# Performance work log

Measured on AMD Instinct MI355X. Metric: run time of the kernel, lower is better.

## Reference

```python
import jax, jax.numpy as jnp
import numpy as np

REG = 0.01          # regularisation (target epsilon)
DECAY = 0.9         # decay_rate
MIN_UPDATE = 0.01   # min_update_size
MAX_ITERS = 50      # max_iterations
GRAD_CLIP = 1.0     # transport_gradient_clip
B, N, D = 4, 2048, 16


@jax.custom_vjp
def clip_grad_identity(t):
    # identity fwd; clips the cotangent of the transport matrix in bwd
    return t

def _cg_fwd(t):
    return t, None

def _cg_bwd(_, dt):
    return (jnp.clip(dt, -GRAD_CLIP, GRAD_CLIP),)

clip_grad_identity.defvjp(_cg_fwd, _cg_bwd)


def _diameter(x):
    # max over dims of per-sample std (ddof=0), per batch -> (B,1)
    d = jnp.max(jnp.std(x, axis=1), axis=-1, keepdims=True)
    return jnp.where(d == 0.0, jnp.ones_like(d), d)


def _sq_cdist(x):
    # squared euclidean auto-distance matrix, (B,N,N)
    sq = jnp.sum(x * x, axis=-1)
    c = sq[:, :, None] + sq[:, None, :] - 2.0 * jnp.einsum('bnd,bmd->bnm', x, x)
    return jnp.maximum(c, 0.0)


def sinkhorn_loop(log_a, log_b, cost, eps_target, min_update, max_iter, eps0, rate):
    """Log-domain Sinkhorn with per-batch exponentially decayed epsilon and
    masked early stopping (data-dependent stop expressed as a convergence mask
    so the loop is jit/vjp friendly). eps0: (B,1,1) initial regularisation
    (extent of the scaled particles, per Thornton & Corenflos)."""
    Bb, _ = log_a.shape
    init = (jnp.zeros_like(log_a), jnp.zeros_like(log_b), eps0,
            jnp.zeros((Bb, 1), dtype=bool))

    @jax.checkpoint
    def step(carry, _):
        f, g, eps, done = carry              # eps: (B,1,1), done: (B,1)
        eps2 = eps[:, :, 0]                  # (B,1)
        # f_i = -eps * LSE_j( log_b_j + (g_j - C_ij)/eps )
        f_new = -eps2 * jax.nn.logsumexp(log_b[:, None, :] + (g[:, None, :] - cost) / eps, axis=-1)
        cT = jnp.swapaxes(cost, 1, 2)
        # g_j = -eps * LSE_i( log_a_i + (f_i - C_ij)/eps )
        g_new = -eps2 * jax.nn.logsumexp(log_a[:, None, :] + (f_new[:, None, :] - cT) / eps, axis=-1)
        upd = jnp.maximum(jnp.max(jnp.abs(f_new - f), axis=-1),
                          jnp.max(jnp.abs(g_new - g), axis=-1))[:, None]  # (B,1)
        converged = (upd < min_update) & (eps2 <= eps_target)
        f = jnp.where(done, f, f_new)
        g = jnp.where(done, g, g_new)
        eps = jnp.where(done[:, :, None], eps, jnp.maximum(eps * rate, eps_target))
        done = done | converged
        return (f, g, eps, done), None

    (f, g, eps, _), _ = jax.lax.scan(step, init, None, length=max_iter)
    return f, g, eps


def _forward(state, weight):
    n = state.shape[1]
    log_b = jnp.full(weight.shape, -jnp.log(float(n)), weight.dtype)  # log uniform
    centred = state - jax.lax.stop_gradient(jnp.mean(state, axis=1, keepdims=True))
    scale = jax.lax.stop_gradient(_diameter(state)) * jnp.sqrt(float(state.shape[-1]))  # (B,1)
    sx = centred / scale[:, :, None]
    cost = _sq_cdist(sx)                                              # (B,N,N)
    extent = (jnp.max(sx, axis=(1, 2)) - jnp.min(sx, axis=(1, 2))).reshape(-1, 1, 1)
    f, g, _ = sinkhorn_loop(weight, log_b, cost, REG, MIN_UPDATE, MAX_ITERS, extent, DECAY)
    # transport from potentials at the target regularisation
    log_T = weight[:, :, None] + log_b[:, None, :] + (f[:, :, None] + g[:, None, :] - cost) / REG
    transport = clip_grad_identity(jnp.exp(log_T))                    # (B,N,N)
    # new particle m = N * sum_n T_nm x_n
    new_state = float(n) * jnp.einsum('bnm,bnd->bmd', transport, state)
    return new_state


def setup_inputs() -> dict:
    key = jax.random.key(0)
    k1, k2 = jax.random.split(key)
    state = jax.random.normal(k1, (B, N, D), dtype=jnp.float32)
    weight = jax.nn.log_softmax(jax.random.normal(k2, (B, N), dtype=jnp.float32), axis=-1)
    return {"state": state, "weight": weight}


def reference(state, weight):
    new_state = _forward(state, weight)
    uniform_log_w = jnp.full(weight.shape, -jnp.log(float(weight.shape[1])), weight.dtype)
    return (new_state, uniform_log_w)
```

## Files before the change

### kernel.cpp

```cpp
#include <hip/hip_runtime.h>

#define BATCH 4
#define NPTS  2048
#define DIM   16
#define REGEPS 0.01f
#define DECAYF 0.9f
#define MINUPD 0.01f
#define MAXIT  50
#define LOGN   7.62461898616f

#define OFF_SX    0
#define OFF_SQ    (BATCH*NPTS*DIM)
#define OFF_F     (OFF_SQ + BATCH*NPTS)
#define OFF_G     (OFF_F + BATCH*NPTS)
#define OFF_MEAN  (OFF_G + BATCH*NPTS)
#define OFF_SCALE (OFF_MEAN + BATCH*DIM)
#define OFF_EPS0  (OFF_SCALE + BATCH)
#define OFF_UPD   (OFF_EPS0 + BATCH)
#define OFF_DONE  (OFF_UPD + BATCH)
#define OFF_CNT   (OFF_DONE + BATCH)

__global__ __launch_bounds__(256) void ot_preproc(const float* __restrict__ state,
                                                  float* __restrict__ ws) {
  const int b = blockIdx.x;
  const int tid = threadIdx.x;
  __shared__ float s_sum[16][17];
  __shared__ float s_sq[16][17];
  __shared__ float s_mean[16];
  __shared__ float s_red[8];
  __shared__ float s_scale_sh;

  const float* st = state + b * NPTS * DIM;
  const int d = tid & 15, grp = tid >> 4;
  float sm = 0.f, s2 = 0.f;
  for (int n = grp; n < NPTS; n += 16) {
    float x = st[n * DIM + d];
    sm += x; s2 += x * x;
  }
  s_sum[grp][d] = sm; s_sq[grp][d] = s2;
  __syncthreads();
  if (tid < 16) {
    float S = 0.f, Q = 0.f;
    for (int g2 = 0; g2 < 16; ++g2) { S += s_sum[g2][tid]; Q += s_sq[g2][tid]; }
    float mean = S * (1.0f / NPTS);
    float var  = fmaxf(Q * (1.0f / NPTS) - mean * mean, 0.f);
    float sd   = sqrtf(var);
    s_mean[tid] = mean;
    ws[OFF_MEAN + b * DIM + tid] = mean;
    s_sum[0][tid] = sd;
  }
  __syncthreads();
  if (tid == 0) {
    float dm = 0.f;
    for (int d2 = 0; d2 < 16; ++d2) dm = fmaxf(dm, s_sum[0][d2]);
    if (dm == 0.f) dm = 1.f;
    float scale = dm * 4.0f;
    s_scale_sh = scale;
    ws[OFF_SCALE + b] = scale;
  }
  __syncthreads();

  const float inv_scale = 1.0f / s_scale_sh;
  float vmin = 3.0e38f, vmax = -3.0e38f;
  float* sx = ws + OFF_SX + b * NPTS * DIM;
  float* sq = ws + OFF_SQ + b * NPTS;
  for (int n = tid; n < NPTS; n += 256) {
    const float4* rp = (const float4*)(st + n * DIM);
    float4 xs0 = rp[0], xs1 = rp[1], xs2 = rp[2], xs3 = rp[3];
    float xv[16] = {xs0.x,xs0.y,xs0.z,xs0.w, xs1.x,xs1.y,xs1.z,xs1.w,
                    xs2.x,xs2.y,xs2.z,xs2.w, xs3.x,xs3.y,xs3.z,xs3.w};
    float ov[16];
    float q = 0.f;
    #pragma unroll
    for (int e = 0; e < 16; ++e) {
      float v = (xv[e] - s_mean[e]) * inv_scale;
      ov[e] = v; q += v * v;
      vmin = fminf(vmin, v); vmax = fmaxf(vmax, v);
    }
    float4* op = (float4*)(sx + n * DIM);
    op[0] = make_float4(ov[0],ov[1],ov[2],ov[3]);
    op[1] = make_float4(ov[4],ov[5],ov[6],ov[7]);
    op[2] = make_float4(ov[8],ov[9],ov[10],ov[11]);
    op[3] = make_float4(ov[12],ov[13],ov[14],ov[15]);
    sq[n] = q;
  }
  float* fv = ws + OFF_F + b * NPTS;
  float* gv = ws + OFF_G + b * NPTS;
  for (int n = tid; n < NPTS; n += 256) { fv[n] = 0.f; gv[n] = 0.f; }
  #pragma unroll
  for (int off = 32; off > 0; off >>= 1) {
    vmin = fminf(vmin, __shfl_xor(vmin, off));
    vmax = fmaxf(vmax, __shfl_xor(vmax, off));
  }
  const int wv = tid >> 6, ln = tid & 63;
  if (ln == 0) { s_red[wv] = vmin; s_red[4 + wv] = vmax; }
  __syncthreads();
  if (tid == 0) {
    float mn = fminf(fminf(s_red[0], s_red[1]), fminf(s_red[2], s_red[3]));
    float mx = fmaxf(fmaxf(s_red[4], s_red[5]), fmaxf(s_red[6], s_red[7]));
    ws[OFF_EPS0 + b] = mx - mn;
    ((unsigned int*)ws)[OFF_UPD + b] = 0u;
    ((int*)ws)[OFF_DONE + b] = 0;
  }
  if (b == 0 && tid < 64) ((int*)ws)[OFF_CNT + tid] = 0;
}

__global__ __launch_bounds__(256) void ot_pass(float* __restrict__ ws,
                                               const float* __restrict__ wlog,
                                               int it, int isF) {
  __shared__ float s_xt[DIM][256];
  __shared__ float s_a[256];
  __shared__ float s_q[256];

  const int bid = blockIdx.x;
  const int b  = bid >> 7;
  const int rb = bid & 127;
  const int tid = threadIdx.x;
  const int w = tid >> 6, l = tid & 63;

  if (!((const int*)ws)[OFF_DONE + b]) {
    float e = ws[OFF_EPS0 + b];
    #pragma unroll 1
    for (int t = 0; t < it; ++t) e = fmaxf(e * DECAYF, REGEPS);
    const float inv_e = 1.0f / e;

    const float* __restrict__ sx = ws + OFF_SX + b * NPTS * DIM;
    const float* __restrict__ sq = ws + OFF_SQ + b * NPTS;
    float* fv = ws + OFF_F + b * NPTS;
    float* gv = ws + OFF_G + b * NPTS;
    const float* __restrict__ wl = wlog + b * NPTS;

    const int row0 = rb * 16 + w * 4;
    float sxi[4][DIM], ci[4], m[4], ssum[4];
    #pragma unroll
    for (int r = 0; r < 4; ++r) {
      const int i = row0 + r;
      ci[r] = sq[i];
      const float4* rp = (const float4*)(sx + i * DIM);
      #pragma unroll
      for (int c4 = 0; c4 < 4; ++c4) {
        float4 t = rp[c4];
        sxi[r][c4*4+0] = -2.0f * t.x; sxi[r][c4*4+1] = -2.0f * t.y;
        sxi[r][c4*4+2] = -2.0f * t.z; sxi[r][c4*4+3] = -2.0f * t.w;
      }
      m[r] = -3.0e38f; ssum[r] = 0.0f;
    }

    const float* __restrict__ src = isF ? gv : fv;
    for (int k = 0; k < NPTS / 256; ++k) {
      __syncthreads();
      {
        const int j = k * 256 + tid;
        const float4* rp = (const float4*)(sx + j * DIM);
        float4 t0 = rp[0], t1 = rp[1], t2 = rp[2], t3 = rp[3];
        s_xt[0][tid]=t0.x;  s_xt[1][tid]=t0.y;  s_xt[2][tid]=t0.z;  s_xt[3][tid]=t0.w;
        s_xt[4][tid]=t1.x;  s_xt[5][tid]=t1.y;  s_xt[6][tid]=t1.z;  s_xt[7][tid]=t1.w;
        s_xt[8][tid]=t2.x;  s_xt[9][tid]=t2.y;  s_xt[10][tid]=t2.z; s_xt[11][tid]=t2.w;
        s_xt[12][tid]=t3.x; s_xt[13][tid]=t3.y; s_xt[14][tid]=t3.z; s_xt[15][tid]=t3.w;
        s_q[tid] = sq[j];
        float aj = src[j] * inv_e;
        if (!isF) aj += wl[j];
        s_a[tid] = aj;
      }
      __syncthreads();
      const float4 av = *(const float4*)&s_a[4 * l];
      const float4 qv = *(const float4*)&s_q[4 * l];
      float acc[4][4];
      #pragma unroll
      for (int r = 0; r < 4; ++r) {
        acc[r][0] = ci[r] + qv.x; acc[r][1] = ci[r] + qv.y;
        acc[r][2] = ci[r] + qv.z; acc[r][3] = ci[r] + qv.w;
      }
      #pragma unroll
      for (int dd = 0; dd < DIM; ++dd) {
        const float4 xj = *(const float4*)&s_xt[dd][4 * l];
        #pragma unroll
        for (int r = 0; r < 4; ++r) {
          const float xr = sxi[r][dd];
          acc[r][0] = fmaf(xr, xj.x, acc[r][0]);
          acc[r][1] = fmaf(xr, xj.y, acc[r][1]);
          acc[r][2] = fmaf(xr, xj.z, acc[r][2]);
          acc[r][3] = fmaf(xr, xj.w, acc[r][3]);
        }
      }
      #pragma unroll
      for (int r = 0; r < 4; ++r) {
        float v0 = fmaf(fmaxf(acc[r][0], 0.0f), -inv_e, av.x);
        float v1 = fmaf(fmaxf(acc[r][1], 0.0f), -inv_e, av.y);
        float v2 = fmaf(fmaxf(acc[r][2], 0.0f), -inv_e, av.z);
        float v3 = fmaf(fmaxf(acc[r][3], 0.0f), -inv_e, av.w);
        float cmx = fmaxf(fmaxf(v0, v1), fmaxf(v2, v3));
        float nm = fmaxf(m[r], cmx);
        float e0 = __expf(m[r] - nm);
        float sadd = __expf(v0-nm) + __expf(v1-nm) + __expf(v2-nm) + __expf(v3-nm);
        ssum[r] = fmaf(ssum[r], e0, sadd);
        m[r] = nm;
      }
    }
    #pragma unroll
    for (int off = 1; off < 64; off <<= 1) {
      #pragma unroll
      for (int r = 0; r < 4; ++r) {
        float om = __shfl_xor(m[r], off);
        float os = __shfl_xor(ssum[r], off);
        float nm = fmaxf(m[r], om);
        ssum[r] = fmaf(ssum[r], __expf(m[r]-nm), os * __expf(om-nm));
        m[r] = nm;
      }
    }
    if (l < 4) {
      const int r = l;
      float L = m[r] + __logf(ssum[r]);
      if (isF) L -= LOGN;
      const float nv = -e * L;
      float* dst = isF ? fv : gv;
      const int i = row0 + r;
      const float old = dst[i];
      dst[i] = nv;
      atomicMax((unsigned int*)ws + OFF_UPD + b, __float_as_uint(fabsf(nv - old)));
    }
  }

  if (!isF) {
    __syncthreads();
    if (tid == 0) {
      __threadfence();
      const int old = atomicAdd((int*)ws + OFF_CNT + it, 1);
      if (old == (int)gridDim.x - 1) {
        __threadfence();
        #pragma unroll 1
        for (int bb = 0; bb < BATCH; ++bb) {
          if (!((int*)ws)[OFF_DONE + bb]) {
            float u = __uint_as_float(atomicMax((unsigned int*)ws + OFF_UPD + bb, 0u));
            float e2 = ws[OFF_EPS0 + bb];
            #pragma unroll 1
            for (int t = 0; t < it; ++t) e2 = fmaxf(e2 * DECAYF, REGEPS);
            if (u < MINUPD && e2 <= REGEPS) ((int*)ws)[OFF_DONE + bb] = 1;
          }
          ((unsigned int*)ws)[OFF_UPD + bb] = 0u;
        }
        __threadfence();
      }
    }
  }
}

__global__ __launch_bounds__(256) void ot_out(float* __restrict__ ws,
                                              const float* __restrict__ wlog,
                                              float* __restrict__ out) {
  __shared__ float s_xt[DIM][256];
  __shared__ float s_p[256];
  __shared__ float s_q[256];
  const int bid = blockIdx.x;
  const int b  = bid >> 8;
  const int rb = bid & 255;
  const int tid = threadIdx.x;
  const int w = tid >> 6, l = tid & 63;
  const float invR = 1.0f / REGEPS;

  const float* __restrict__ sx = ws + OFF_SX + b * NPTS * DIM;
  const float* __restrict__ sq = ws + OFF_SQ + b * NPTS;
  const float* __restrict__ fv = ws + OFF_F + b * NPTS;
  const float* __restrict__ gv = ws + OFF_G + b * NPTS;
  const float* __restrict__ wl = wlog + b * NPTS;

  const int row0 = rb * 8 + w * 2;
  float sxm[2][DIM], cm2[2], qm[2], acc[2][DIM], accT[2];
  #pragma unroll
  for (int r = 0; r < 2; ++r) {
    const int mrow = row0 + r;
    cm2[r] = sq[mrow];
    qm[r]  = gv[mrow] * invR;
    const float4* rp = (const float4*)(sx + mrow * DIM);
    #pragma unroll
    for (int c4 = 0; c4 < 4; ++c4) {
      float4 t = rp[c4];
      sxm[r][c4*4+0] = -2.0f * t.x; sxm[r][c4*4+1] = -2.0f * t.y;
      sxm[r][c4*4+2] = -2.0f * t.z; sxm[r][c4*4+3] = -2.0f * t.w;
    }
    #pragma unroll
    for (int dd = 0; dd < DIM; ++dd) acc[r][dd] = 0.0f;
    accT[r] = 0.0f;
  }

  for (int k = 0; k < NPTS / 256; ++k) {
    __syncthreads();
    {
      const int n = k * 256 + tid;
      const float4* rp = (const float4*)(sx + n * DIM);
      float4 t0 = rp[0], t1 = rp[1], t2 = rp[2], t3 = rp[3];
      s_xt[0][tid]=t0.x;  s_xt[1][tid]=t0.y;  s_xt[2][tid]=t0.z;  s_xt[3][tid]=t0.w;
      s_xt[4][tid]=t1.x;  s_xt[5][tid]=t1.y;  s_xt[6][tid]=t1.z;  s_xt[7][tid]=t1.w;
      s_xt[8][tid]=t2.x;  s_xt[9][tid]=t2.y;  s_xt[10][tid]=t2.z; s_xt[11][tid]=t2.w;
      s_xt[12][tid]=t3.x; s_xt[13][tid]=t3.y; s_xt[14][tid]=t3.z; s_xt[15][tid]=t3.w;
      s_q[tid] = sq[n];
      s_p[tid] = wl[n] - LOGN + fv[n] * invR;
    }
    __syncthreads();
    const float4 pv = *(const float4*)&s_p[4 * l];
    const float4 qv = *(const float4*)&s_q[4 * l];
    float a2[2][4];
    #pragma unroll
    for (int r = 0; r < 2; ++r) {
      a2[r][0] = cm2[r] + qv.x; a2[r][1] = cm2[r] + qv.y;
      a2[r][2] = cm2[r] + qv.z; a2[r][3] = cm2[r] + qv.w;
    }
    #pragma unroll
    for (int dd = 0; dd < DIM; ++dd) {
      const float4 xj = *(const float4*)&s_xt[dd][4 * l];
      #pragma unroll
      for (int r = 0; r < 2; ++r) {
        const float xr = sxm[r][dd];
        a2[r][0] = fmaf(xr, xj.x, a2[r][0]);
        a2[r][1] = fmaf(xr, xj.y, a2[r][1]);
        a2[r][2] = fmaf(xr, xj.z, a2[r][2]);
        a2[r][3] = fmaf(xr, xj.w, a2[r][3]);
      }
    }
    float T[2][4];
    #pragma unroll
    for (int r = 0; r < 2; ++r) {
      T[r][0] = __expf(fmaf(fmaxf(a2[r][0], 0.f), -invR, pv.x + qm[r]));
      T[r][1] = __expf(fmaf(fmaxf(a2[r][1], 0.f), -invR, pv.y + qm[r]));
      T[r][2] = __expf(fmaf(fmaxf(a2[r][2], 0.f), -invR, pv.z + qm[r]));
      T[r][3] = __expf(fmaf(fmaxf(a2[r][3], 0.f), -invR, pv.w + qm[r]));
      accT[r] += (T[r][0] + T[r][1]) + (T[r][2] + T[r][3]);
    }
    #pragma unroll
    for (int dd = 0; dd < DIM; ++dd) {
      const float4 xj = *(const float4*)&s_xt[dd][4 * l];
      #pragma unroll
      for (int r = 0; r < 2; ++r) {
        float t = acc[r][dd];
        t = fmaf(T[r][0], xj.x, t);
        t = fmaf(T[r][1], xj.y, t);
        t = fmaf(T[r][2], xj.z, t);
        t = fmaf(T[r][3], xj.w, t);
        acc[r][dd] = t;
      }
    }
  }
  #pragma unroll
  for (int off = 1; off < 64; off <<= 1) {
    #pragma unroll
    for (int r = 0; r < 2; ++r) {
      #pragma unroll
      for (int dd = 0; dd < DIM; ++dd) acc[r][dd] += __shfl_xor(acc[r][dd], off);
      accT[r] += __shfl_xor(accT[r], off);
    }
  }
  if (l == 0) {
    const float scale = ws[OFF_SCALE + b];
    const float* mean = ws + OFF_MEAN + b * DIM;
    #pragma unroll
    for (int r = 0; r < 2; ++r) {
      const int mrow = row0 + r;
      float ov[16];
      #pragma unroll
      for (int dd = 0; dd < DIM; ++dd)
        ov[dd] = (float)NPTS * fmaf(scale, acc[r][dd], mean[dd] * accT[r]);
      float4* op = (float4*)(out + (b * NPTS + mrow) * DIM);
      op[0] = make_float4(ov[0],ov[1],ov[2],ov[3]);
      op[1] = make_float4(ov[4],ov[5],ov[6],ov[7]);
      op[2] = make_float4(ov[8],ov[9],ov[10],ov[11]);
      op[3] = make_float4(ov[12],ov[13],ov[14],ov[15]);
    }
  }
  if (tid < 8) out[BATCH * NPTS * DIM + b * NPTS + rb * 8 + tid] = -LOGN;
}

extern "C" void kernel_launch(void* const* d_in, const int* in_sizes, int n_in,
                              void* d_out, int out_size, void* d_ws, size_t ws_size,
                              hipStream_t stream) {
  (void)in_sizes; (void)n_in; (void)out_size; (void)ws_size;
  const float* state  = (const float*)d_in[0];
  const float* weight = (const float*)d_in[1];
  float* out = (float*)d_out;
  float* ws  = (float*)d_ws;

  ot_preproc<<<dim3(BATCH), dim3(256), 0, stream>>>(state, ws);
  for (int it = 0; it < MAXIT; ++it) {
    ot_pass<<<dim3(BATCH * NPTS / 16), dim3(256), 0, stream>>>(ws, weight, it, 1);
    ot_pass<<<dim3(BATCH * NPTS / 16), dim3(256), 0, stream>>>(ws, weight, it, 0);
  }
  ot_out<<<dim3(BATCH * NPTS / 8), dim3(256), 0, stream>>>(ws, weight, out);
}
```

Baseline: 4.105 ms.

## Fuse Sinkhorn iterations into one persistent cooperative kernel with per-batch grid barriers

Measured after the change: 7.464 ms. +81.9%, slower.

```diff
diff --git a/kernel.cpp b/kernel.cpp
--- a/kernel.cpp
+++ b/kernel.cpp
@@ -8,6 +8,8 @@
 #define MINUPD 0.01f
 #define MAXIT  50
 #define LOGN   7.62461898616f
+#define L2E    1.44269504089f
+#define LN2    0.69314718056f
 
 #define OFF_SX    0
 #define OFF_SQ    (BATCH*NPTS*DIM)
@@ -16,9 +18,8 @@
 #define OFF_MEAN  (OFF_G + BATCH*NPTS)
 #define OFF_SCALE (OFF_MEAN + BATCH*DIM)
 #define OFF_EPS0  (OFF_SCALE + BATCH)
-#define OFF_UPD   (OFF_EPS0 + BATCH)
-#define OFF_DONE  (OFF_UPD + BATCH)
-#define OFF_CNT   (OFF_DONE + BATCH)
+#define OFF_ARR   (OFF_EPS0 + BATCH)
+#define OFF_UPD2  (OFF_ARR + BATCH)
 
 __global__ __launch_bounds__(256) void ot_preproc(const float* __restrict__ state,
                                                   float* __restrict__ ws) {
@@ -99,148 +100,207 @@
     float mn = fminf(fminf(s_red[0], s_red[1]), fminf(s_red[2], s_red[3]));
     float mx = fmaxf(fmaxf(s_red[4], s_red[5]), fmaxf(s_red[6], s_red[7]));
     ws[OFF_EPS0 + b] = mx - mn;
-    ((unsigned int*)ws)[OFF_UPD + b] = 0u;
-    ((int*)ws)[OFF_DONE + b] = 0;
-  }
-  if (b == 0 && tid < 64) ((int*)ws)[OFF_CNT + tid] = 0;
-}
-
-__global__ __launch_bounds__(256) void ot_pass(float* __restrict__ ws,
-                                               const float* __restrict__ wlog,
-                                               int it, int isF) {
-  __shared__ float s_xt[DIM][256];
-  __shared__ float s_a[256];
-  __shared__ float s_q[256];
+    ((unsigned int*)ws)[OFF_UPD2 + 2*b + 0] = 0u;
+    ((unsigned int*)ws)[OFF_UPD2 + 2*b + 1] = 0u;
+    ((int*)ws)[OFF_ARR + b] = 0;
+  }
+}
+
+__device__ __forceinline__ void batch_barrier(int* arr, int target) {
+  __syncthreads();
+  if (threadIdx.x == 0) {
+    __hip_atomic_fetch_add(arr, 1, __ATOMIC_ACQ_REL, __HIP_MEMORY_SCOPE_AGENT);
+    while (__hip_atomic_load(arr, __ATOMIC_ACQUIRE, __HIP_MEMORY_SCOPE_AGENT) < target)
+      __builtin_amdgcn_s_sleep(8);
+  }
+  __syncthreads();
+}
+
+__device__ __forceinline__ void lse_sweep(const float* __restrict__ s_xt,
+                                          const float* __restrict__ s_a2,
+                                          const float (&sxs)[4][16],
+                                          float (&M)[4], float (&S)[4], int l) {
+  #pragma unroll
+  for (int r = 0; r < 4; ++r) { M[r] = -3.0e38f; S[r] = 0.0f; }
+  for (int c = 0; c < 8; ++c) {
+    const int jb = c * 256 + 4 * l;
+    const float4 av = *(const float4*)(s_a2 + jb);
+    float acc[4][4];
+    {
+      const float4 xj = *(const float4*)(s_xt + jb);
+      #pragma unroll
+      for (int r = 0; r < 4; ++r) {
+        acc[r][0] = fmaf(sxs[r][0], xj.x, av.x);
+        acc[r][1] = fmaf(sxs[r][0], xj.y, av.y);
+        acc[r][2] = fmaf(sxs[r][0], xj.z, av.z);
+        acc[r][3] = fmaf(sxs[r][0], xj.w, av.w);
+      }
+    }
+    #pragma unroll
+    for (int dd = 1; dd < 16; ++dd) {
+      const float4 xj = *(const float4*)(s_xt + dd * 2048 + jb);
+      #pragma unroll
+      for (int r = 0; r < 4; ++r) {
+        acc[r][0] = fmaf(sxs[r][dd], xj.x, acc[r][0]);
+        acc[r][1] = fmaf(sxs[r][dd], xj.y, acc[r][1]);
+        acc[r][2] = fmaf(sxs[r][dd], xj.z, acc[r][2]);
+        acc[r][3] = fmaf(sxs[r][dd], xj.w, acc[r][3]);
+      }
+    }
+    #pragma unroll
+    for (int r = 0; r < 4; ++r) {
+      const float cmx = fmaxf(fmaxf(acc[r][0], acc[r][1]), fmaxf(acc[r][2], acc[r][3]));
+      const float nm = fmaxf(M[r], cmx);
+      const float e0 = exp2f(M[r] - nm);
+      const float sa = exp2f(acc[r][0]-nm) + exp2f(acc[r][1]-nm)
+                     + exp2f(acc[r][2]-nm) + exp2f(acc[r][3]-nm);
+      S[r] = fmaf(S[r], e0, sa);
+      M[r] = nm;
+    }
+  }
+}
+
+__device__ __forceinline__ void lse_butterfly(float (&M)[4], float (&S)[4]) {
+  #pragma unroll
+  for (int off = 1; off < 64; off <<= 1) {
+    #pragma unroll
+    for (int r = 0; r < 4; ++r) {
+      const float om = __shfl_xor(M[r], off);
+      const float os = __shfl_xor(S[r], off);
+      const float nm = fmaxf(M[r], om);
+      S[r] = S[r] * exp2f(M[r] - nm) + os * exp2f(om - nm);
+      M[r] = nm;
+    }
+  }
+}
+
+__global__ __launch_bounds__(512, 2) void ot_sinkhorn(float* __restrict__ ws,
+                                                      const float* __restrict__ wlog) {
+  extern __shared__ float lds[];
+  float* s_xt  = lds;
+  float* s_a2  = lds + 16 * 2048;
+  float* s_wl2 = s_a2 + 2048;
 
   const int bid = blockIdx.x;
-  const int b  = bid >> 7;
-  const int rb = bid & 127;
+  const int b  = bid >> 6;
+  const int rb = bid & 63;
   const int tid = threadIdx.x;
   const int w = tid >> 6, l = tid & 63;
 
-  if (!((const int*)ws)[OFF_DONE + b]) {
-    float e = ws[OFF_EPS0 + b];
-    #pragma unroll 1
-    for (int t = 0; t < it; ++t) e = fmaxf(e * DECAYF, REGEPS);
-    const float inv_e = 1.0f / e;
-
-    const float* __restrict__ sx = ws + OFF_SX + b * NPTS * DIM;
-    const float* __restrict__ sq = ws + OFF_SQ + b * NPTS;
-    float* fv = ws + OFF_F + b * NPTS;
-    float* gv = ws + OFF_G + b * NPTS;
-    const float* __restrict__ wl = wlog + b * NPTS;
-
-    const int row0 = rb * 16 + w * 4;
-    float sxi[4][DIM], ci[4], m[4], ssum[4];
-    #pragma unroll
-    for (int r = 0; r < 4; ++r) {
-      const int i = row0 + r;
-      ci[r] = sq[i];
-      const float4* rp = (const float4*)(sx + i * DIM);
-      #pragma unroll
-      for (int c4 = 0; c4 < 4; ++c4) {
-        float4 t = rp[c4];
-        sxi[r][c4*4+0] = -2.0f * t.x; sxi[r][c4*4+1] = -2.0f * t.y;
-        sxi[r][c4*4+2] = -2.0f * t.z; sxi[r][c4*4+3] = -2.0f * t.w;
-      }
-      m[r] = -3.0e38f; ssum[r] = 0.0f;
-    }
-
-    const float* __restrict__ src = isF ? gv : fv;
-    for (int k = 0; k < NPTS / 256; ++k) {
-      __syncthreads();
-      {
-        const int j = k * 256 + tid;
-        const float4* rp = (const float4*)(sx + j * DIM);
-        float4 t0 = rp[0], t1 = rp[1], t2 = rp[2], t3 = rp[3];
-        s_xt[0][tid]=t0.x;  s_xt[1][tid]=t0.y;  s_xt[2][tid]=t0.z;  s_xt[3][tid]=t0.w;
-        s_xt[4][tid]=t1.x;  s_xt[5][tid]=t1.y;  s_xt[6][tid]=t1.z;  s_xt[7][tid]=t1.w;
-        s_xt[8][tid]=t2.x;  s_xt[9][tid]=t2.y;  s_xt[10][tid]=t2.z; s_xt[11][tid]=t2.w;
-        s_xt[12][tid]=t3.x; s_xt[13][tid]=t3.y; s_xt[14][tid]=t3.z; s_xt[15][tid]=t3.w;
-        s_q[tid] = sq[j];
-        float aj = src[j] * inv_e;
-        if (!isF) aj += wl[j];
-        s_a[tid] = aj;
-      }
-      __syncthreads();
-      const float4 av = *(const float4*)&s_a[4 * l];
-      const float4 qv = *(const float4*)&s_q[4 * l];
-      float acc[4][4];
-      #pragma unroll
-      for (int r = 0; r < 4; ++r) {
-        acc[r][0] = ci[r] + qv.x; acc[r][1] = ci[r] + qv.y;
-        acc[r][2] = ci[r] + qv.z; acc[r][3] = ci[r] + qv.w;
-      }
-      #pragma unroll
-      for (int dd = 0; dd < DIM; ++dd) {
-        const float4 xj = *(const float4*)&s_xt[dd][4 * l];
+  const float* __restrict__ sx = ws + OFF_SX + b * NPTS * DIM;
+  const float* __restrict__ sq = ws + OFF_SQ + b * NPTS;
+  float* fv = ws + OFF_F + b * NPTS;
+  float* gv = ws + OFF_G + b * NPTS;
+  const float* __restrict__ wl = wlog + b * NPTS;
+  int* arr = (int*)ws + OFF_ARR + b;
+  unsigned int* up2 = (unsigned int*)ws + OFF_UPD2 + 2 * b;
+
+  for (int j = tid; j < NPTS; j += 512) {
+    const float4* rp = (const float4*)(sx + j * DIM);
+    float4 t0 = rp[0], t1 = rp[1], t2 = rp[2], t3 = rp[3];
+    s_xt[ 0*2048+j]=t0.x; s_xt[ 1*2048+j]=t0.y; s_xt[ 2*2048+j]=t0.z; s_xt[ 3*2048+j]=t0.w;
+    s_xt[ 4*2048+j]=t1.x; s_xt[ 5*2048+j]=t1.y; s_xt[ 6*2048+j]=t1.z; s_xt[ 7*2048+j]=t1.w;
+    s_xt[ 8*2048+j]=t2.x; s_xt[ 9*2048+j]=t2.y; s_xt[10*2048+j]=t2.z; s_xt[11*2048+j]=t2.w;
+    s_xt[12*2048+j]=t3.x; s_xt[13*2048+j]=t3.y; s_xt[14*2048+j]=t3.z; s_xt[15*2048+j]=t3.w;
+    s_wl2[j] = wl[j] * L2E;
+  }
+  const int row0 = rb * 32 + w * 4;
+  float sxs[4][16];
+  #pragma unroll
+  for (int r = 0; r < 4; ++r) {
+    const float4* rp = (const float4*)(sx + (row0 + r) * DIM);
+    float4 t0 = rp[0], t1 = rp[1], t2 = rp[2], t3 = rp[3];
+    sxs[r][0]=t0.x;  sxs[r][1]=t0.y;  sxs[r][2]=t0.z;  sxs[r][3]=t0.w;
+    sxs[r][4]=t1.x;  sxs[r][5]=t1.y;  sxs[r][6]=t1.z;  sxs[r][7]=t1.w;
+    sxs[r][8]=t2.x;  sxs[r][9]=t2.y;  sxs[r][10]=t2.z; sxs[r][11]=t2.w;
+    sxs[r][12]=t3.x; sxs[r][13]=t3.y; sxs[r][14]=t3.z; sxs[r][15]=t3.w;
+  }
+  float eps = ws[OFF_EPS0 + b];
+  {
+    const float s2e0 = 2.0f * L2E / eps;
+    #pragma unroll
+    for (int r = 0; r < 4; ++r)
+      #pragma unroll
+      for (int dd = 0; dd < 16; ++dd) sxs[r][dd] *= s2e0;
+  }
+  __syncthreads();
+
+  int ph = 0;
+  for (int it = 0; it < MAXIT; ++it) {
+    const float le   = L2E / eps;
+    const float eln2 = eps * LN2;
+
+    {
+      const int j4 = tid * 4;
+      const float g0 = __hip_atomic_load(gv + j4 + 0, __ATOMIC_RELAXED, __HIP_MEMORY_SCOPE_AGENT);
+      const float g1 = __hip_atomic_load(gv + j4 + 1, __ATOMIC_RELAXED, __HIP_MEMORY_SCOPE_AGENT);
+      const float g2 = __hip_atomic_load(gv + j4 + 2, __ATOMIC_RELAXED, __HIP_MEMORY_SCOPE_AGENT);
+      const float g3 = __hip_atomic_load(gv + j4 + 3, __ATOMIC_RELAXED, __HIP_MEMORY_SCOPE_AGENT);
+      const float4 qj = *(const float4*)(sq + j4);
+      *(float4*)(s_a2 + j4) = make_float4((g0 - qj.x) * le, (g1 - qj.y) * le,
+                                          (g2 - qj.z) * le, (g3 - qj.w) * le);
+    }
+    __syncthreads();
+    {
+      float M[4], S[4];
+      lse_sweep(s_xt, s_a2, sxs, M, S, l);
+      lse_butterfly(M, S);
+      if (l < 4) {
+        const float Mr = (l==0)?M[0]:(l==1)?M[1]:(l==2)?M[2]:M[3];
+        const float Sr = (l==0)?S[0]:(l==1)?S[1]:(l==2)?S[2]:S[3];
+        const int i = row0 + l;
+        const float qi = sq[i];
+        const float fnew = fmaf(eps, LOGN, qi) - eln2 * (Mr + log2f(Sr));
+        const float old = __hip_atomic_load(fv + i, __ATOMIC_RELAXED, __HIP_MEMORY_SCOPE_AGENT);
+        __hip_atomic_store(fv + i, fnew, __ATOMIC_RELEASE, __HIP_MEMORY_SCOPE_AGENT);
+        __hip_atomic_fetch_max(up2 + (it & 1), __float_as_uint(fabsf(fnew - old)),
+                               __ATOMIC_RELAXED, __HIP_MEMORY_SCOPE_AGENT);
+      }
+    }
+    ++ph; batch_barrier(arr, 64 * ph);
+
+    if (rb == 0 && tid == 0)
+      __hip_atomic_store(up2 + ((it + 1) & 1), 0u, __ATOMIC_RELAXED, __HIP_MEMORY_SCOPE_AGENT);
+    {
+      const int j4 = tid * 4;
+      const float f0 = __hip_atomic_load(fv + j4 + 0, __ATOMIC_RELAXED, __HIP_MEMORY_SCOPE_AGENT);
+      const float f1 = __hip_atomic_load(fv + j4 + 1, __ATOMIC_RELAXED, __HIP_MEMORY_SCOPE_AGENT);
+      const float f2 = __hip_atomic_load(fv + j4 + 2, __ATOMIC_RELAXED, __HIP_MEMORY_SCOPE_AGENT);
+      const float f3 = __hip_atomic_load(fv + j4 + 3, __ATOMIC_RELAXED, __HIP_MEMORY_SCOPE_AGENT);
+      const float4 qj = *(const float4*)(sq + j4);
+      const float4 w2 = *(const float4*)(s_wl2 + j4);
+      *(float4*)(s_a2 + j4) = make_float4(fmaf(f0 - qj.x, le, w2.x), fmaf(f1 - qj.y, le, w2.y),
+                                          fmaf(f2 - qj.z, le, w2.z), fmaf(f3 - qj.w, le, w2.w));
+    }
+    __syncthreads();
+    {
+      float M[4], S[4];
+      lse_sweep(s_xt, s_a2, sxs, M, S, l);
+      lse_butterfly(M, S);
+      if (l < 4) {
+        const float Mr = (l==0)?M[0]:(l==1)?M[1]:(l==2)?M[2]:M[3];
+        const float Sr = (l==0)?S[0]:(l==1)?S[1]:(l==2)?S[2]:S[3];
+        const int i = row0 + l;
+        const float qm = sq[i];
+        const float gnew = qm - eln2 * (Mr + log2f(Sr));
+        const float old = __hip_atomic_load(gv + i, __ATOMIC_RELAXED, __HIP_MEMORY_SCOPE_AGENT);
+        __hip_atomic_store(gv + i, gnew, __ATOMIC_RELEASE, __HIP_MEMORY_SCOPE_AGENT);
+        __hip_atomic_fetch_max(up2 + (it & 1), __float_as_uint(fabsf(gnew - old)),
+                               __ATOMIC_RELAXED, __HIP_MEMORY_SCOPE_AGENT);
+      }
+    }
+    if (it < MAXIT - 1) {
+      ++ph; batch_barrier(arr, 64 * ph);
+      const unsigned uu = __hip_atomic_load(up2 + (it & 1), __ATOMIC_RELAXED, __HIP_MEMORY_SCOPE_AGENT);
+      const bool conv = (__uint_as_float(uu) < MINUPD) && (eps <= REGEPS);
+      if (conv) break;
+      const float en = fmaxf(eps * DECAYF, REGEPS);
+      const float ratio = eps / en;
+      eps = en;
+      #pragma unroll
+      for (int r = 0; r < 4; ++r)
         #pragma unroll
-        for (int r = 0; r < 4; ++r) {
-          const float xr = sxi[r][dd];
-          acc[r][0] = fmaf(xr, xj.x, acc[r][0]);
-          acc[r][1] = fmaf(xr, xj.y, acc[r][1]);
-          acc[r][2] = fmaf(xr, xj.z, acc[r][2]);
-          acc[r][3] = fmaf(xr, xj.w, acc[r][3]);
-        }
-      }
-      #pragma unroll
-      for (int r = 0; r < 4; ++r) {
-        float v0 = fmaf(fmaxf(acc[r][0], 0.0f), -inv_e, av.x);
-        float v1 = fmaf(fmaxf(acc[r][1], 0.0f), -inv_e, av.y);
-        float v2 = fmaf(fmaxf(acc[r][2], 0.0f), -inv_e, av.z);
-        float v3 = fmaf(fmaxf(acc[r][3], 0.0f), -inv_e, av.w);
-        float cmx = fmaxf(fmaxf(v0, v1), fmaxf(v2, v3));
-        float nm = fmaxf(m[r], cmx);
-        float e0 = __expf(m[r] - nm);
-        float sadd = __expf(v0-nm) + __expf(v1-nm) + __expf(v2-nm) + __expf(v3-nm);
-        ssum[r] = fmaf(ssum[r], e0, sadd);
-        m[r] = nm;
-      }
-    }
-    #pragma unroll
-    for (int off = 1; off < 64; off <<= 1) {
-      #pragma unroll
-      for (int r = 0; r < 4; ++r) {
-        float om = __shfl_xor(m[r], off);
-        float os = __shfl_xor(ssum[r], off);
-        float nm = fmaxf(m[r], om);
-        ssum[r] = fmaf(ssum[r], __expf(m[r]-nm), os * __expf(om-nm));
-        m[r] = nm;
-      }
-    }
-    if (l < 4) {
-      const int r = l;
-      float L = m[r] + __logf(ssum[r]);
-      if (isF) L -= LOGN;
-      const float nv = -e * L;
-      float* dst = isF ? fv : gv;
-      const int i = row0 + r;
-      const float old = dst[i];
-      dst[i] = nv;
-      atomicMax((unsigned int*)ws + OFF_UPD + b, __float_as_uint(fabsf(nv - old)));
-    }
-  }
-
-  if (!isF) {
-    __syncthreads();
-    if (tid == 0) {
-      __threadfence();
-      const int old = atomicAdd((int*)ws + OFF_CNT + it, 1);
-      if (old == (int)gridDim.x - 1) {
-        __threadfence();
-        #pragma unroll 1
-        for (int bb = 0; bb < BATCH; ++bb) {
-          if (!((int*)ws)[OFF_DONE + bb]) {
-            float u = __uint_as_float(atomicMax((unsigned int*)ws + OFF_UPD + bb, 0u));
-            float e2 = ws[OFF_EPS0 + bb];
-            #pragma unroll 1
-            for (int t = 0; t < it; ++t) e2 = fmaxf(e2 * DECAYF, REGEPS);
-            if (u < MINUPD && e2 <= REGEPS) ((int*)ws)[OFF_DONE + bb] = 1;
-          }
-          ((unsigned int*)ws)[OFF_UPD + bb] = 0u;
-        }
-        __threadfence();
-      }
+        for (int dd = 0; dd < 16; ++dd) sxs[r][dd] *= ratio;
     }
   }
 }
@@ -379,9 +439,19 @@
   float* ws  = (float*)d_ws;
 
   ot_preproc<<<dim3(BATCH), dim3(256), 0, stream>>>(state, ws);
-  for (int it = 0; it < MAXIT; ++it) {
-    ot_pass<<<dim3(BATCH * NPTS / 16), dim3(256), 0, stream>>>(ws, weight, it, 1);
-    ot_pass<<<dim3(BATCH * NPTS / 16), dim3(256), 0, stream>>>(ws, weight, it, 0);
-  }
+
+  const unsigned int dynLds = 147456;
+  hipFuncSetAttribute((const void*)ot_sinkhorn,
+                      hipFuncAttributeMaxDynamicSharedMemorySize, (int)dynLds);
+  {
+    float* wsf = ws;
+    const float* wgt = weight;
+    void* ka[2] = { (void*)&wsf, (void*)&wgt };
+    if (hipLaunchCooperativeKernel((const void*)ot_sinkhorn, dim3(256), dim3(512),
+                                   ka, dynLds, stream) != hipSuccess) {
+      hipLaunchKernelGGL(ot_sinkhorn, dim3(256), dim3(512), dynLds, stream, ws, weight);
+    }
+  }
+
   ot_out<<<dim3(BATCH * NPTS / 8), dim3(256), 0, stream>>>(ws, weight, out);
 }
```
